# Kernel optimization log

Measured on AMD Instinct MI355X. Metric: run time of the kernel, lower is better.

The kernel has to match this reference:

```python
import jax, jax.numpy as jnp
import numpy as np

NEG = jnp.float32(-1e30)  # max-plus identity (finite to keep grads clean)


def setup_inputs() -> dict:
    key = jax.random.key(0)
    k1, k2 = jax.random.split(key)
    B, Cin, H, W = 8, 64, 64, 64
    Cout, kH, kW = 64, 3, 3
    x = jax.random.normal(k1, (B, Cin, H, W), dtype=jnp.float32)
    weight = jax.random.normal(k2, (Cout, Cin, kH, kW), dtype=jnp.float32)
    return {"x": x, "weight": weight, "kernel_size": 3, "padding": 1}


def reference(x, weight, kernel_size, padding):
    # Max-plus correlation (tropical conv), stride 1:
    #   out[b,co,y,x] = max_{ci,i,j} ( x_pad[b,ci,y+i,x+j] + weight[co,ci,i,j] )
    kH = kW = int(kernel_size)
    padH = padW = int(padding)
    B, Cin, H, W = x.shape
    Cout = weight.shape[0]
    xp = jnp.pad(x, ((0, 0), (0, 0), (padH, padH), (padW, padW)),
                 constant_values=NEG)  # -inf-like padding: identity of max
    Ho = H + 2 * padH - kH + 1
    Wo = W + 2 * padW - kW + 1
    out = jnp.full((B, Cout, Ho, Wo), NEG, dtype=x.dtype)
    for i in range(kH):          # small fixed kernel loop (kH*kW taps)
        for j in range(kW):
            win = xp[:, :, i:i + Ho, j:j + Wo]            # [B,Ci,Ho,Wo]
            cand = win[:, None] + weight[None, :, :, i, j, None, None]
            out = jnp.maximum(out, cand.max(axis=2))      # reduce over Ci
    return out
```

## Files before the change

kernel.cpp:

```cpp
#include <hip/hip_runtime.h>

#define NEGV -1e30f

constexpr int Bn = 8, Ci = 64, Hn = 64, Wn = 64, Co = 64;

constexpr int G  = 4;
constexpr int CW = Wn / G;

__global__ __launch_bounds__(256)
void wtrans_kernel(const float* __restrict__ wt, float* __restrict__ wT) {
    int idx = blockIdx.x * 256 + threadIdx.x;
    if (idx < Ci * 9 * Co) {
        int co = idx & 63;
        int k  = (idx >> 6) % 9;
        int ci = idx / (9 * Co);
        wT[idx] = wt[((size_t)co * Ci + ci) * 9 + k];
    }
}

__device__ __forceinline__ float vmax3(float a, float b, float c) {
    float d;
    asm("v_max3_f32 %0, %1, %2, %3" : "=v"(d) : "v"(a), "v"(b), "v"(c));
    return d;
}

template<int EDGE>
__device__ __forceinline__ void load6(float* xv, const float* __restrict__ p) {
    if (EDGE == 1) {
        xv[0] = NEGV;
#pragma unroll
        for (int c = 1; c < 6; c++) xv[c] = p[c - 1];
    } else if (EDGE == 2) {
#pragma unroll
        for (int c = 0; c < 5; c++) xv[c] = p[c];
        xv[5] = NEGV;
    } else {
#pragma unroll
        for (int c = 0; c < 6; c++) xv[c] = p[c];
    }
}

struct Win { float u[6], c[6], d[6]; };

template<int EDGE>
__device__ __forceinline__ void loadwin(Win& w, const float* __restrict__ px,
                                        bool hasUp, bool hasDn) {
    load6<EDGE>(w.c, px);
    if (hasUp) load6<EDGE>(w.u, px - Wn);
    else {
#pragma unroll
        for (int c = 0; c < 6; c++) w.u[c] = NEGV;
    }
    if (hasDn) load6<EDGE>(w.d, px + Wn);
    else {
#pragma unroll
        for (int c = 0; c < 6; c++) w.d[c] = NEGV;
    }
}

__device__ __forceinline__ void loadw(float* wv, const float* __restrict__ wrow,
                                      int lane) {
#pragma unroll
    for (int k = 0; k < 9; k++) wv[k] = wrow[k * Co + lane];
}

__device__ __forceinline__ void compute(float* a, const Win& w, const float* wv) {
#pragma unroll
    for (int p = 0; p < G; p++) {
        float t0 = w.u[p] + wv[0], t1 = w.u[p + 1] + wv[1], t2 = w.u[p + 2] + wv[2];
        float t3 = w.c[p] + wv[3], t4 = w.c[p + 1] + wv[4], t5 = w.c[p + 2] + wv[5];
        float t6 = w.d[p] + wv[6], t7 = w.d[p + 1] + wv[7], t8 = w.d[p + 2] + wv[8];
        float m0 = vmax3(t0, t1, t2);
        float m1 = vmax3(t3, t4, t5);
        float m2 = vmax3(t6, t7, t8);
        a[p] = vmax3(a[p], m0, m1);
        a[p] = fmaxf(a[p], m2);
    }
}

template<int EDGE>
__device__ __forceinline__ void run_wave(const float* __restrict__ x,
                                         const float* __restrict__ wT,
                                         float* __restrict__ out,
                                         int b, int h, int w0, int lane) {
    const bool hasUp = (h > 0);
    const bool hasDn = (h < Hn - 1);
    const int  cb    = (EDGE == 1) ? 0 : (w0 - 1);

    const float* px   = x + (((size_t)b * Ci) * Hn + h) * Wn + cb;
    const float* wrow = wT;

    float a[G];
#pragma unroll
    for (int p = 0; p < G; p++) a[p] = NEGV;

    Win wA, wB;
    float vA[9], vB[9];

    loadw(vA, wrow, lane);  wrow += 9 * Co;

#pragma unroll 1
    for (int ci = 0; ci < Ci - 2; ci += 2) {
        loadw(vB, wrow, lane);  wrow += 9 * Co;
        loadwin<EDGE>(wA, px, hasUp, hasDn);  px += Hn * Wn;
        compute(a, wA, vA);
        loadw(vA, wrow, lane);  wrow += 9 * Co;
        loadwin<EDGE>(wB, px, hasUp, hasDn);  px += Hn * Wn;
        compute(a, wB, vB);
    }
    loadw(vB, wrow, lane);
    loadwin<EDGE>(wA, px, hasUp, hasDn);  px += Hn * Wn;
    compute(a, wA, vA);
    loadwin<EDGE>(wB, px, hasUp, hasDn);
    compute(a, wB, vB);

    float4 st = make_float4(a[0], a[1], a[2], a[3]);
    *reinterpret_cast<float4*>(out + (((size_t)b * Co + lane) * Hn + h) * Wn + w0) = st;
}

__global__ __launch_bounds__(256, 8)
void maxconv_main(const float* __restrict__ x, const float* __restrict__ wT,
                  float* __restrict__ out) {
    const int lane = threadIdx.x & 63;
    const int wid  = threadIdx.x >> 6;
    const int cw   = __builtin_amdgcn_readfirstlane(blockIdx.x * 4 + wid);
    const int w0   = cw * G;
    const int h    = blockIdx.y;
    const int b    = blockIdx.z;

    if (cw == 0)           run_wave<1>(x, wT, out, b, h, w0, lane);
    else if (cw == CW - 1) run_wave<2>(x, wT, out, b, h, w0, lane);
    else                   run_wave<0>(x, wT, out, b, h, w0, lane);
}

extern "C" void kernel_launch(void* const* d_in, const int* in_sizes, int n_in,
                              void* d_out, int out_size, void* d_ws, size_t ws_size,
                              hipStream_t stream) {
    const float* x  = (const float*)d_in[0];
    const float* wt = (const float*)d_in[1];
    float* out = (float*)d_out;
    float* wT  = (float*)d_ws;

    wtrans_kernel<<<(Ci * 9 * Co + 255) / 256, 256, 0, stream>>>(wt, wT);

    dim3 grid(CW / 4, Hn, Bn);
    maxconv_main<<<grid, 256, 0, stream>>>(x, wT, out);
}
```

Before: 122.0 us.

## Widen per-wave output tile to 8 columns, prefetch windows, remap block order

Each wave now computes 8 output columns instead of 4. The weights loaded per input channel are reused across twice as many outputs, which halves the weight-load traffic per output. The input window loads are software-pipelined one channel ahead, with explicit lgkmcnt drains and scheduling barriers, to overlap scalar loads with compute. The launch becomes a 1D grid of 1024 blocks, remapped so blocks handling nearby rows are interleaved, presumably for cache locality. The costs are more registers and lower occupancy (launch bounds drop to 4 blocks), plus half as many blocks in total.

```diff
diff --git a/kernel.cpp b/kernel.cpp
--- a/kernel.cpp
+++ b/kernel.cpp
@@ -4,7 +4,7 @@
 
 constexpr int Bn = 8, Ci = 64, Hn = 64, Wn = 64, Co = 64;
 
-constexpr int G  = 4;
+constexpr int G  = 8;
 constexpr int CW = Wn / G;
 
 __global__ __launch_bounds__(256)
@@ -25,36 +25,36 @@
 }
 
 template<int EDGE>
-__device__ __forceinline__ void load6(float* xv, const float* __restrict__ p) {
+__device__ __forceinline__ void load10(float* xv, const float* __restrict__ p) {
     if (EDGE == 1) {
         xv[0] = NEGV;
 #pragma unroll
-        for (int c = 1; c < 6; c++) xv[c] = p[c - 1];
+        for (int c = 1; c < 10; c++) xv[c] = p[c - 1];
     } else if (EDGE == 2) {
 #pragma unroll
-        for (int c = 0; c < 5; c++) xv[c] = p[c];
-        xv[5] = NEGV;
+        for (int c = 0; c < 9; c++) xv[c] = p[c];
+        xv[9] = NEGV;
     } else {
 #pragma unroll
-        for (int c = 0; c < 6; c++) xv[c] = p[c];
+        for (int c = 0; c < 10; c++) xv[c] = p[c];
     }
 }
 
-struct Win { float u[6], c[6], d[6]; };
+struct Win { float u[10], c[10], d[10]; };
 
 template<int EDGE>
 __device__ __forceinline__ void loadwin(Win& w, const float* __restrict__ px,
                                         bool hasUp, bool hasDn) {
-    load6<EDGE>(w.c, px);
-    if (hasUp) load6<EDGE>(w.u, px - Wn);
+    load10<EDGE>(w.c, px);
+    if (hasUp) load10<EDGE>(w.u, px - Wn);
     else {
 #pragma unroll
-        for (int c = 0; c < 6; c++) w.u[c] = NEGV;
+        for (int c = 0; c < 10; c++) w.u[c] = NEGV;
     }
-    if (hasDn) load6<EDGE>(w.d, px + Wn);
+    if (hasDn) load10<EDGE>(w.d, px + Wn);
     else {
 #pragma unroll
-        for (int c = 0; c < 6; c++) w.d[c] = NEGV;
+        for (int c = 0; c < 10; c++) w.d[c] = NEGV;
     }
 }
 
@@ -78,6 +78,11 @@
     }
 }
 
+#define SMEM_DRAIN() do {                                   \
+    asm volatile("s_waitcnt lgkmcnt(0)" ::: "memory");      \
+    __builtin_amdgcn_sched_barrier(0);                      \
+} while (0)
+
 template<int EDGE>
 __device__ __forceinline__ void run_wave(const float* __restrict__ x,
                                          const float* __restrict__ wT,
@@ -98,35 +103,51 @@
     float vA[9], vB[9];
 
     loadw(vA, wrow, lane);  wrow += 9 * Co;
+    loadwin<EDGE>(wA, px, hasUp, hasDn);  px += Hn * Wn;
 
 #pragma unroll 1
     for (int ci = 0; ci < Ci - 2; ci += 2) {
+        SMEM_DRAIN();
+        loadwin<EDGE>(wB, px, hasUp, hasDn);  px += Hn * Wn;
+        __builtin_amdgcn_sched_barrier(0);
         loadw(vB, wrow, lane);  wrow += 9 * Co;
+        compute(a, wA, vA);
+
+        SMEM_DRAIN();
         loadwin<EDGE>(wA, px, hasUp, hasDn);  px += Hn * Wn;
-        compute(a, wA, vA);
+        __builtin_amdgcn_sched_barrier(0);
         loadw(vA, wrow, lane);  wrow += 9 * Co;
-        loadwin<EDGE>(wB, px, hasUp, hasDn);  px += Hn * Wn;
         compute(a, wB, vB);
     }
+    SMEM_DRAIN();
+    loadwin<EDGE>(wB, px, hasUp, hasDn);
+    __builtin_amdgcn_sched_barrier(0);
     loadw(vB, wrow, lane);
-    loadwin<EDGE>(wA, px, hasUp, hasDn);  px += Hn * Wn;
     compute(a, wA, vA);
-    loadwin<EDGE>(wB, px, hasUp, hasDn);
+    SMEM_DRAIN();
     compute(a, wB, vB);
 
-    float4 st = make_float4(a[0], a[1], a[2], a[3]);
-    *reinterpret_cast<float4*>(out + (((size_t)b * Co + lane) * Hn + h) * Wn + w0) = st;
+    float* po = out + (((size_t)b * Co + lane) * Hn + h) * Wn + w0;
+    *reinterpret_cast<float4*>(po)     = make_float4(a[0], a[1], a[2], a[3]);
+    *reinterpret_cast<float4*>(po + 4) = make_float4(a[4], a[5], a[6], a[7]);
 }
 
-__global__ __launch_bounds__(256, 8)
+__global__ __launch_bounds__(256, 4)
 void maxconv_main(const float* __restrict__ x, const float* __restrict__ wT,
                   float* __restrict__ out) {
     const int lane = threadIdx.x & 63;
     const int wid  = threadIdx.x >> 6;
-    const int cw   = __builtin_amdgcn_readfirstlane(blockIdx.x * 4 + wid);
+
+    const int id   = blockIdx.x;
+    const int band = id & 7;
+    const int t    = id >> 3;
+    const int bx   = t & 1;
+    const int u    = t >> 1;
+    const int h    = band * 8 + (u & 7);
+    const int b    = u >> 3;
+
+    const int cw   = __builtin_amdgcn_readfirstlane(bx * 4 + wid);
     const int w0   = cw * G;
-    const int h    = blockIdx.y;
-    const int b    = blockIdx.z;
 
     if (cw == 0)           run_wave<1>(x, wT, out, b, h, w0, lane);
     else if (cw == CW - 1) run_wave<2>(x, wT, out, b, h, w0, lane);
@@ -143,6 +164,5 @@
 
     wtrans_kernel<<<(Ci * 9 * Co + 255) / 256, 256, 0, stream>>>(wt, wT);
 
-    dim3 grid(CW / 4, Hn, Bn);
-    maxconv_main<<<grid, 256, 0, stream>>>(x, wT, out);
+    maxconv_main<<<1024, 256, 0, stream>>>(x, wT, out);
 }
```

Measured after the change: 120.4 us. Within noise of the previous version (-1.3%).
